# Kernel optimization log

Measured on AMD Instinct MI355X. Metric: run time of the kernel, lower is better.

The kernel has to match this reference:

```python
import jax, jax.numpy as jnp
import numpy as np

N_NODES = 1024
N_MARBLES = 3072
N = N_NODES + N_MARBLES
N_EATERS = 64
DIM = 2
EPS = 1e-6


def setup_inputs() -> dict:
    key = jax.random.key(0)
    k1, k2, k3, k4, k5 = jax.random.split(key, 5)
    positions = jax.random.normal(k1, (N, DIM), dtype=jnp.float32) * 10.0
    velocities = jax.random.normal(k2, (N, DIM), dtype=jnp.float32)
    masses = jax.random.uniform(k3, (N,), dtype=jnp.float32) + 0.1  # strictly positive
    eater_idx = jax.random.randint(k4, (N_EATERS,), 0, N_NODES)
    eater_radius = jax.random.uniform(k5, (N_EATERS,), dtype=jnp.float32) * 0.5
    dt = jnp.ones((1,), dtype=jnp.float32) * 0.01
    return {"positions": positions, "velocities": velocities, "masses": masses,
            "eater_idx": eater_idx, "eater_radius": eater_radius, "dt": dt}


def reference(positions, velocities, masses, eater_idx, eater_radius, dt):
    # --- all-pairs net force (vectorized form of __compute_net_force_for) ---
    diff = positions[None, :, :] - positions[:, None, :]          # [N, N, D], r_j - r_i
    dist2 = jnp.sum(diff * diff, axis=-1)                          # [N, N]
    safe_d2 = jnp.where(dist2 > 0, dist2, 1.0)
    inv_d3 = jnp.where(dist2 > 0, (safe_d2 + EPS) ** -1.5, 0.0)    # excludes self (j == i)
    # gravity-style attraction: F_i = sum_j m_i m_j (r_j - r_i) / |r_j - r_i|^3
    force = jnp.einsum('i,j,ij,ijd->id', masses, masses, inv_d3, diff)  # [N, D]

    # --- update_acceleration + update_movement (semi-implicit Euler) ---
    acc = force / masses[:, None]
    vel_new = velocities + acc * dt                                # dt broadcasts from [1]
    pos_new = positions + vel_new * dt

    # --- __feed_marble_if_close_to_any_eater ---
    marble_pos = pos_new[N_NODES:]                                 # [M, D]
    eater_pos = pos_new[eater_idx]                                 # [E, D]
    d2 = jnp.sum((marble_pos[:, None, :] - eater_pos[None, :, :]) ** 2, axis=-1)  # [M, E]
    eaten = jnp.any(d2 <= (eater_radius[None, :] ** 2), axis=1)    # [M] bool

    state_new = jnp.stack([pos_new, vel_new])                      # [2, N, D]
    return state_new, eaten
```

## Files before the change

### kernel.cpp

```cpp
#include <hip/hip_runtime.h>

#define N_TOTAL   4096
#define N_NODES   1024
#define N_MARBLES 3072
#define N_EATERS  64
#define EPS       1e-6f
#define BLOCK     256
#define JCHUNK    64
#define JCHUNKS   (N_TOTAL / JCHUNK)

__global__ __launch_bounds__(BLOCK) void force_partial(
    const float2* __restrict__ pos2, const float* __restrict__ mass,
    float2* __restrict__ partial)
{
    const int i  = blockIdx.x * BLOCK + threadIdx.x;
    const int j0 = blockIdx.y * JCHUNK;

    const float2 pi = pos2[i];
    float ax = 0.f, ay = 0.f;

#pragma unroll 16
    for (int j = j0; j < j0 + JCHUNK; ++j) {
        const float2 pj = pos2[j];
        const float dx = pj.x - pi.x;
        const float dy = pj.y - pi.y;
        const float t  = fmaf(dx, dx, fmaf(dy, dy, EPS));
        const float r  = rsqrtf(t);
        const float w  = r * r * r * mass[j];
        ax = fmaf(w, dx, ax);
        ay = fmaf(w, dy, ay);
    }

    partial[blockIdx.y * N_TOTAL + i] = make_float2(ax, ay);
}

__global__ __launch_bounds__(BLOCK) void integrate(
    const float2* __restrict__ pos2, const float2* __restrict__ vel2,
    const float2* __restrict__ partial, const float* __restrict__ dtp,
    float2* __restrict__ out2)
{
    __shared__ float2 red[4][64];

    const int lane = threadIdx.x & 63;
    const int w    = threadIdx.x >> 6;
    const int i    = blockIdx.x * 64 + lane;

    float ax = 0.f, ay = 0.f;
#pragma unroll 16
    for (int jc = w * 16; jc < w * 16 + 16; ++jc) {
        const float2 p = partial[jc * N_TOTAL + i];
        ax += p.x;
        ay += p.y;
    }
    red[w][lane] = make_float2(ax, ay);
    __syncthreads();

    if (w == 0) {
        const float2 r1 = red[1][lane];
        const float2 r2 = red[2][lane];
        const float2 r3 = red[3][lane];
        ax += r1.x + r2.x + r3.x;
        ay += r1.y + r2.y + r3.y;

        const float dt = dtp[0];
        const float2 v = vel2[i];
        const float2 p = pos2[i];
        const float vx = v.x + ax * dt;
        const float vy = v.y + ay * dt;
        const float px = p.x + vx * dt;
        const float py = p.y + vy * dt;

        out2[i]           = make_float2(px, py);
        out2[N_TOTAL + i] = make_float2(vx, vy);
    }
}

__global__ __launch_bounds__(BLOCK) void eaten_kernel(
    const float2* __restrict__ out_pos2, const int* __restrict__ eater_idx,
    const float* __restrict__ eater_radius, float* __restrict__ out_eaten)
{
    __shared__ float ex[N_EATERS], ey[N_EATERS], er2[N_EATERS];
    if (threadIdx.x < N_EATERS) {
        const float2 ep = out_pos2[eater_idx[threadIdx.x]];
        ex[threadIdx.x] = ep.x;
        ey[threadIdx.x] = ep.y;
        const float r = eater_radius[threadIdx.x];
        er2[threadIdx.x] = r * r;
    }
    __syncthreads();

    const int m = blockIdx.x * blockDim.x + threadIdx.x;
    const float2 mp = out_pos2[N_NODES + m];

    bool any = false;
#pragma unroll
    for (int e = 0; e < N_EATERS; ++e) {
        const float dx = mp.x - ex[e];
        const float dy = mp.y - ey[e];
        any = any || (dx * dx + dy * dy <= er2[e]);
    }
    out_eaten[m] = any ? 1.0f : 0.0f;
}

extern "C" void kernel_launch(void* const* d_in, const int* in_sizes, int n_in,
                              void* d_out, int out_size, void* d_ws, size_t ws_size,
                              hipStream_t stream) {
    const float* pos  = (const float*)d_in[0];
    const float* vel  = (const float*)d_in[1];
    const float* mass = (const float*)d_in[2];
    const int*   eidx = (const int*)d_in[3];
    const float* erad = (const float*)d_in[4];
    const float* dt   = (const float*)d_in[5];

    float* out      = (float*)d_out;
    float2* partial = (float2*)d_ws;

    dim3 g1(N_TOTAL / BLOCK, JCHUNKS);
    force_partial<<<g1, BLOCK, 0, stream>>>((const float2*)pos, mass, partial);
    integrate<<<N_TOTAL / 64, BLOCK, 0, stream>>>(
        (const float2*)pos, (const float2*)vel, partial, dt, (float2*)out);
    eaten_kernel<<<N_MARBLES / BLOCK, BLOCK, 0, stream>>>(
        (const float2*)out, eidx, erad, out + 4 * N_TOTAL);
}
```

Measured before the change: 77.22 us.

## Fuse eaten check into integrate kernel and pack two bodies per thread

```diff
diff --git a/kernel.cpp b/kernel.cpp
--- a/kernel.cpp
+++ b/kernel.cpp
@@ -9,41 +9,58 @@
 #define JCHUNK    64
 #define JCHUNKS   (N_TOTAL / JCHUNK)
 
+typedef float v2f __attribute__((ext_vector_type(2)));
+
 __global__ __launch_bounds__(BLOCK) void force_partial(
     const float2* __restrict__ pos2, const float* __restrict__ mass,
     float2* __restrict__ partial)
 {
-    const int i  = blockIdx.x * BLOCK + threadIdx.x;
+    const int i0 = blockIdx.x * (2 * BLOCK) + threadIdx.x;
+    const int i1 = i0 + BLOCK;
     const int j0 = blockIdx.y * JCHUNK;
 
-    const float2 pi = pos2[i];
-    float ax = 0.f, ay = 0.f;
+    const float2 pA = pos2[i0];
+    const float2 pB = pos2[i1];
+    const v2f pix = { pA.x, pB.x };
+    const v2f piy = { pA.y, pB.y };
+
+    v2f ax = { 0.f, 0.f };
+    v2f ay = { 0.f, 0.f };
 
 #pragma unroll 16
     for (int j = j0; j < j0 + JCHUNK; ++j) {
         const float2 pj = pos2[j];
-        const float dx = pj.x - pi.x;
-        const float dy = pj.y - pi.y;
-        const float t  = fmaf(dx, dx, fmaf(dy, dy, EPS));
-        const float r  = rsqrtf(t);
-        const float w  = r * r * r * mass[j];
-        ax = fmaf(w, dx, ax);
-        ay = fmaf(w, dy, ay);
+        const float  mj = mass[j];
+        const v2f dx = pj.x - pix;
+        const v2f dy = pj.y - piy;
+        const v2f t  = dx * dx + (dy * dy + EPS);
+        v2f r;
+        r.x = rsqrtf(t.x);
+        r.y = rsqrtf(t.y);
+        const v2f w = r * r * r * mj;
+        ax += w * dx;
+        ay += w * dy;
     }
 
-    partial[blockIdx.y * N_TOTAL + i] = make_float2(ax, ay);
+    const int row = blockIdx.y * N_TOTAL;
+    partial[row + i0] = make_float2(ax.x, ay.x);
+    partial[row + i1] = make_float2(ax.y, ay.y);
 }
 
-__global__ __launch_bounds__(BLOCK) void integrate(
+__global__ __launch_bounds__(BLOCK) void integrate_eaten(
     const float2* __restrict__ pos2, const float2* __restrict__ vel2,
     const float2* __restrict__ partial, const float* __restrict__ dtp,
-    float2* __restrict__ out2)
+    const int* __restrict__ eater_idx, const float* __restrict__ eater_radius,
+    float2* __restrict__ out2, float* __restrict__ out_eaten)
 {
     __shared__ float2 red[4][64];
+    __shared__ float2 ered[4][64];
+    __shared__ float  exs[N_EATERS], eys[N_EATERS], er2s[N_EATERS];
 
-    const int lane = threadIdx.x & 63;
-    const int w    = threadIdx.x >> 6;
-    const int i    = blockIdx.x * 64 + lane;
+    const int  lane       = threadIdx.x & 63;
+    const int  w          = threadIdx.x >> 6;
+    const int  i          = blockIdx.x * 64 + lane;
+    const bool marble_blk = (blockIdx.x >= N_NODES / 64);
 
     float ax = 0.f, ay = 0.f;
 #pragma unroll 16
@@ -53,7 +70,23 @@
         ay += p.y;
     }
     red[w][lane] = make_float2(ax, ay);
+
+    int q = 0;
+    if (marble_blk) {
+        q = eater_idx[lane];
+        float bx = 0.f, by = 0.f;
+#pragma unroll 16
+        for (int jc = w * 16; jc < w * 16 + 16; ++jc) {
+            const float2 p = partial[jc * N_TOTAL + q];
+            bx += p.x;
+            by += p.y;
+        }
+        ered[w][lane] = make_float2(bx, by);
+    }
     __syncthreads();
+
+    const float dt = dtp[0];
+    float px = 0.f, py = 0.f;
 
     if (w == 0) {
         const float2 r1 = red[1][lane];
@@ -62,44 +95,43 @@
         ax += r1.x + r2.x + r3.x;
         ay += r1.y + r2.y + r3.y;
 
-        const float dt = dtp[0];
         const float2 v = vel2[i];
         const float2 p = pos2[i];
         const float vx = v.x + ax * dt;
         const float vy = v.y + ay * dt;
-        const float px = p.x + vx * dt;
-        const float py = p.y + vy * dt;
+        px = p.x + vx * dt;
+        py = p.y + vy * dt;
 
         out2[i]           = make_float2(px, py);
         out2[N_TOTAL + i] = make_float2(vx, vy);
     }
-}
 
-__global__ __launch_bounds__(BLOCK) void eaten_kernel(
-    const float2* __restrict__ out_pos2, const int* __restrict__ eater_idx,
-    const float* __restrict__ eater_radius, float* __restrict__ out_eaten)
-{
-    __shared__ float ex[N_EATERS], ey[N_EATERS], er2[N_EATERS];
-    if (threadIdx.x < N_EATERS) {
-        const float2 ep = out_pos2[eater_idx[threadIdx.x]];
-        ex[threadIdx.x] = ep.x;
-        ey[threadIdx.x] = ep.y;
-        const float r = eater_radius[threadIdx.x];
-        er2[threadIdx.x] = r * r;
+    if (marble_blk && w == 1) {
+        const float eax = ered[0][lane].x + ered[1][lane].x +
+                          ered[2][lane].x + ered[3][lane].x;
+        const float eay = ered[0][lane].y + ered[1][lane].y +
+                          ered[2][lane].y + ered[3][lane].y;
+        const float2 ev = vel2[q];
+        const float2 ep = pos2[q];
+        const float evx = ev.x + eax * dt;
+        const float evy = ev.y + eay * dt;
+        exs[lane] = ep.x + evx * dt;
+        eys[lane] = ep.y + evy * dt;
+        const float r = eater_radius[lane];
+        er2s[lane] = r * r;
     }
     __syncthreads();
 
-    const int m = blockIdx.x * blockDim.x + threadIdx.x;
-    const float2 mp = out_pos2[N_NODES + m];
-
-    bool any = false;
+    if (marble_blk && w == 0) {
+        bool any = false;
 #pragma unroll
-    for (int e = 0; e < N_EATERS; ++e) {
-        const float dx = mp.x - ex[e];
-        const float dy = mp.y - ey[e];
-        any = any || (dx * dx + dy * dy <= er2[e]);
+        for (int e = 0; e < N_EATERS; ++e) {
+            const float dx = px - exs[e];
+            const float dy = py - eys[e];
+            any = any || (dx * dx + dy * dy <= er2s[e]);
+        }
+        out_eaten[i - N_NODES] = any ? 1.0f : 0.0f;
     }
-    out_eaten[m] = any ? 1.0f : 0.0f;
 }
 
 extern "C" void kernel_launch(void* const* d_in, const int* in_sizes, int n_in,
@@ -115,10 +147,9 @@
     float* out      = (float*)d_out;
     float2* partial = (float2*)d_ws;
 
-    dim3 g1(N_TOTAL / BLOCK, JCHUNKS);
+    dim3 g1(N_TOTAL / (2 * BLOCK), JCHUNKS);
     force_partial<<<g1, BLOCK, 0, stream>>>((const float2*)pos, mass, partial);
-    integrate<<<N_TOTAL / 64, BLOCK, 0, stream>>>(
-        (const float2*)pos, (const float2*)vel, partial, dt, (float2*)out);
-    eaten_kernel<<<N_MARBLES / BLOCK, BLOCK, 0, stream>>>(
-        (const float2*)out, eidx, erad, out + 4 * N_TOTAL);
+    integrate_eaten<<<N_TOTAL / 64, BLOCK, 0, stream>>>(
+        (const float2*)pos, (const float2*)vel, partial, dt,
+        eidx, erad, (float2*)out, out + 4 * N_TOTAL);
 }
```

After: 79.05 us. 2.4% more time.
